# Kernel tuning notes

Measured on AMD Instinct MI355X. Metric: run time of the kernel, lower is better.

Reference implementation:

```python
import jax, jax.numpy as jnp
import numpy as np

B, N, C, O, K, D = 32, 2048, 64, 64, 3, 16

def setup_inputs() -> dict:
    key = jax.random.key(0)
    ks = jax.random.split(key, 6)
    x = jax.random.normal(ks[0], (B, N, C), dtype=jnp.float32)
    node_embeddings = jax.random.normal(ks[1], (N, D), dtype=jnp.float32)
    adj_m = jax.random.uniform(ks[2], (N, N), dtype=jnp.float32)
    weights_pool = jax.random.normal(ks[3], (D, K, C, O), dtype=jnp.float32) * 0.1
    bias_pool = jax.random.normal(ks[4], (D, O), dtype=jnp.float32) * 0.1
    sa_weight = jax.random.normal(ks[5], (N, 2 * N), dtype=jnp.float32) * (1.0 / np.sqrt(2 * N))
    return {"x": x, "node_embeddings": node_embeddings, "adj_m": adj_m,
            "weights_pool": weights_pool, "bias_pool": bias_pool, "sa_weight": sa_weight}

def reference(x, node_embeddings, adj_m, weights_pool, bias_pool, sa_weight):
    n = node_embeddings.shape[0]
    # learned adaptive adjacency [N,N]
    supports = jax.nn.softmax(jax.nn.relu(node_embeddings @ node_embeddings.T), axis=1)
    # SpatialAttention: 1x1 conv over 2N channels == matmul with [N,2N] weight
    z = jnp.concatenate([supports, adj_m], axis=1) @ sa_weight.T  # [N,N]
    s2 = jax.nn.sigmoid(z)
    supports = s2 * adj_m + (1.0 - s2) * supports
    # Chebyshev polynomial basis
    support_set = [jnp.eye(n, dtype=supports.dtype), supports]
    for _ in range(2, K):
        support_set.append(2.0 * supports @ support_set[-1] - support_set[-2])
    supports_k = jnp.stack(support_set, axis=0)  # [K,N,N]
    # per-node generated weights/bias from embeddings
    weights = jnp.einsum('nd,dkio->nkio', node_embeddings, weights_pool)  # [N,K,C,O]
    bias = node_embeddings @ bias_pool  # [N,O]
    # graph conv: aggregate then per-node matmul
    x_g = jnp.einsum('knm,bmc->bnkc', supports_k, x)  # [B,N,K,C]
    x_gconv = jnp.einsum('bnki,nkio->bno', x_g, weights) + bias  # [B,N,O]
    return x_gconv
```

## Files before the change

### kernel.cpp

```cpp
#include <hip/hip_runtime.h>


typedef unsigned short u16;
typedef float f32x4 __attribute__((ext_vector_type(4)));
typedef __bf16 bf16x8 __attribute__((ext_vector_type(8)));
typedef unsigned short u16x8 __attribute__((ext_vector_type(8)));

#define PSTRIDE ((size_t)2048 * 2048)

__device__ __forceinline__ u16 f2bf(float f) {
    unsigned u = __float_as_uint(f);
    u += 0x7FFFu + ((u >> 16) & 1u);
    return (u16)(u >> 16);
}
__device__ __forceinline__ float bf2f(u16 h) {
    return __uint_as_float((unsigned)h << 16);
}
__device__ __forceinline__ void gl_lds16(const void* g, void* l) {
    __builtin_amdgcn_global_load_lds(
        (const __attribute__((address_space(1))) unsigned*)g,
        (__attribute__((address_space(3))) unsigned*)l, 16, 0, 0);
}

__global__ __launch_bounds__(256)
void zsm(const float* __restrict__ E, u16* __restrict__ Acat) {
    __shared__ float Et[16 * 2048];
    __shared__ float redm[4][8], reds[4][8];
    const int tid = threadIdx.x;
    const int r0 = blockIdx.x * 8;

#pragma unroll
    for (int k = 0; k < 8; ++k) {
        const int n = tid + 256 * k;
        const float4* Er = (const float4*)(E + (size_t)n * 16);
        float4 e0 = Er[0], e1 = Er[1], e2 = Er[2], e3 = Er[3];
        Et[0 * 2048 + n] = e0.x;  Et[1 * 2048 + n] = e0.y;
        Et[2 * 2048 + n] = e0.z;  Et[3 * 2048 + n] = e0.w;
        Et[4 * 2048 + n] = e1.x;  Et[5 * 2048 + n] = e1.y;
        Et[6 * 2048 + n] = e1.z;  Et[7 * 2048 + n] = e1.w;
        Et[8 * 2048 + n] = e2.x;  Et[9 * 2048 + n] = e2.y;
        Et[10 * 2048 + n] = e2.z; Et[11 * 2048 + n] = e2.w;
        Et[12 * 2048 + n] = e3.x; Et[13 * 2048 + n] = e3.y;
        Et[14 * 2048 + n] = e3.z; Et[15 * 2048 + n] = e3.w;
    }
    __syncthreads();

    float z[8][8] = {};
#pragma unroll
    for (int d = 0; d < 16; ++d) {
        const float* row = Et + d * 2048;
        float ev[8];
#pragma unroll
        for (int k = 0; k < 8; ++k) ev[k] = row[tid + 256 * k];
#pragma unroll
        for (int r = 0; r < 8; ++r) {
            float e = row[r0 + r];
#pragma unroll
            for (int k = 0; k < 8; ++k) z[r][k] = fmaf(e, ev[k], z[r][k]);
        }
    }
    float mr[8];
#pragma unroll
    for (int r = 0; r < 8; ++r) {
        float m = 0.f;
#pragma unroll
        for (int k = 0; k < 8; ++k) { z[r][k] = fmaxf(z[r][k], 0.f); m = fmaxf(m, z[r][k]); }
        mr[r] = m;
    }
#pragma unroll
    for (int off = 32; off; off >>= 1)
#pragma unroll
        for (int r = 0; r < 8; ++r) mr[r] = fmaxf(mr[r], __shfl_xor(mr[r], off, 64));
    if ((tid & 63) == 0) {
#pragma unroll
        for (int r = 0; r < 8; ++r) redm[tid >> 6][r] = mr[r];
    }
    __syncthreads();
#pragma unroll
    for (int r = 0; r < 8; ++r)
        mr[r] = fmaxf(fmaxf(redm[0][r], redm[1][r]), fmaxf(redm[2][r], redm[3][r]));
    float sr[8];
#pragma unroll
    for (int r = 0; r < 8; ++r) {
        float s = 0.f;
#pragma unroll
        for (int k = 0; k < 8; ++k) { z[r][k] = __expf(z[r][k] - mr[r]); s += z[r][k]; }
        sr[r] = s;
    }
#pragma unroll
    for (int off = 32; off; off >>= 1)
#pragma unroll
        for (int r = 0; r < 8; ++r) sr[r] += __shfl_xor(sr[r], off, 64);
    if ((tid & 63) == 0) {
#pragma unroll
        for (int r = 0; r < 8; ++r) reds[tid >> 6][r] = sr[r];
    }
    __syncthreads();
#pragma unroll
    for (int r = 0; r < 8; ++r) {
        float inv = 1.f / (reds[0][r] + reds[1][r] + reds[2][r] + reds[3][r]);
        u16* orow = Acat + (size_t)(r0 + r) * 4096;
#pragma unroll
        for (int k = 0; k < 8; ++k) orow[tid + 256 * k] = f2bf(z[r][k] * inv);
    }
}

__global__ __launch_bounds__(256)
void convk(const float* __restrict__ adj, const float* __restrict__ saw,
           u16* __restrict__ Acat, u16* __restrict__ sawb) {
    const size_t NADJ = 1048576, STRIDE = (size_t)1536 * 256;
    const size_t e0 = (size_t)blockIdx.x * 256 + threadIdx.x;
    float4 v[8];
#pragma unroll
    for (int it = 0; it < 8; ++it) {
        size_t idx = e0 + (size_t)it * STRIDE;
        const float* src = (idx < NADJ) ? (adj + idx * 4) : (saw + (idx - NADJ) * 4);
        v[it] = *(const float4*)src;
    }
#pragma unroll
    for (int it = 0; it < 8; ++it) {
        size_t idx = e0 + (size_t)it * STRIDE;
        ushort4 o = make_ushort4(f2bf(v[it].x), f2bf(v[it].y), f2bf(v[it].z), f2bf(v[it].w));
        if (idx < NADJ) {
            size_t j = idx * 4;
            int n = (int)(j >> 11), c = (int)(j & 2047);
            *(ushort4*)(Acat + (size_t)n * 4096 + 2048 + c) = o;
        } else {
            *(ushort4*)(sawb + (idx - NADJ) * 4) = o;
        }
    }
}

__global__ __launch_bounds__(256)
void preamble(const float* __restrict__ E, const float* __restrict__ x,
              const float* __restrict__ Wp, const float* __restrict__ bp,
              u16* __restrict__ xtT, u16* __restrict__ Wpb, float* __restrict__ Wpbf,
              float* __restrict__ bias, u16* __restrict__ xn, int mode) {
    __shared__ float tw[64][193];
    __shared__ u16 t[64][65];
    const int bid = blockIdx.x, tid = threadIdx.x;

    if (bid < 16) {
        const int d = bid;
        const float* base = Wp + (size_t)d * 12288;
        const int o = tid & 63, seg = tid >> 6;
#pragma unroll
        for (int j = 0; j < 48; ++j) {
            int ki = seg * 48 + j;
            int k = ki >> 6, i = ki & 63;
            float v;
            if (k == 0)      v = base[i * 64 + o] - base[8192 + i * 64 + o];
            else if (k == 1) v = base[4096 + i * 64 + o];
            else             v = 2.f * base[8192 + i * 64 + o];
            tw[o][ki] = v;
        }
        __syncthreads();
#pragma unroll
        for (int it = 0; it < 12; ++it) {
            int idx = tid + it * 256;
            int oo = idx / 48, q = idx - oo * 48;
            float v0 = tw[oo][q * 4], v1 = tw[oo][q * 4 + 1];
            float v2 = tw[oo][q * 4 + 2], v3 = tw[oo][q * 4 + 3];
            size_t dst = (size_t)(d * 64 + oo) * 192 + q * 4;
            *(float4*)(Wpbf + dst) = make_float4(v0, v1, v2, v3);
            *(ushort4*)(Wpb + dst) = make_ushort4(f2bf(v0), f2bf(v1), f2bf(v2), f2bf(v3));
        }
    } else if (bid < 80) {
        const int nb = bid - 16;
#pragma unroll
        for (int it = 0; it < 8; ++it) {
            int idx = tid + it * 256;
            int n = nb * 32 + (idx >> 6), o = idx & 63;
            float s = 0.f;
#pragma unroll
            for (int d = 0; d < 16; ++d) s = fmaf(E[n * 16 + d], bp[d * 64 + o], s);
            bias[(size_t)n * 64 + o] = s;
        }
    } else {
        int local = bid - 80;
        int m0 = (local & 31) * 64, b = local >> 5;
        int c = tid & 63, g = tid >> 6;
#pragma unroll
        for (int r = 0; r < 16; ++r) {
            int mm = g * 16 + r;
            t[mm][c] = f2bf(x[((size_t)b * 2048 + m0 + mm) * 64 + c]);
        }
        __syncthreads();
#pragma unroll
        for (int r = 0; r < 16; ++r) {
            int cc = g * 16 + r;
            xtT[((size_t)b * 64 + cc) * 2048 + m0 + c] = t[c][cc];
        }
        if (mode) {
#pragma unroll
            for (int r = 0; r < 16; ++r) {
                int mm = g * 16 + r;
                xn[((size_t)(m0 + mm)) * 2048 + b * 64 + c] = t[mm][c];
            }
        }
    }
}

__global__ __launch_bounds__(256)
void mid(const float* __restrict__ E, const float* __restrict__ Wpbf,
         u16* __restrict__ Wnb) {
    __shared__ float Es[32 * 16];
    const int w = blockIdx.x, tid = threadIdx.x;
    const int c0 = (w % 12) * 1024, n0 = (w / 12) * 32;
    for (int j = tid; j < 512; j += 256) Es[j] = E[(size_t)n0 * 16 + j];
    float4 wf[16];
#pragma unroll
    for (int d = 0; d < 16; ++d)
        wf[d] = *(const float4*)(Wpbf + (size_t)d * 12288 + c0 + tid * 4);
    __syncthreads();
    for (int nl = 0; nl < 32; ++nl) {
        float4 s = make_float4(0.f, 0.f, 0.f, 0.f);
#pragma unroll
        for (int d = 0; d < 16; ++d) {
            float e = Es[nl * 16 + d];
            s.x = fmaf(e, wf[d].x, s.x);
            s.y = fmaf(e, wf[d].y, s.y);
            s.z = fmaf(e, wf[d].z, s.z);
            s.w = fmaf(e, wf[d].w, s.w);
        }
        *(ushort4*)(Wnb + (size_t)(n0 + nl) * 12288 + c0 + tid * 4) =
            make_ushort4(f2bf(s.x), f2bf(s.y), f2bf(s.z), f2bf(s.w));
    }
}

__global__ __launch_bounds__(512, 2)
void gemm_bt256(const u16* __restrict__ A, const u16* __restrict__ Bt,
                u16* __restrict__ Cp, int M, int N, int K, int Kh) {
    __shared__ alignas(16) u16 As[2][256 * 64];
    __shared__ alignas(16) u16 Bs[2][256 * 64];
    const int tid = threadIdx.x, lane = tid & 63, wave = tid >> 6;

    const int nbx = gridDim.x, nby = gridDim.y, nbz = gridDim.z;
    const int nwg = nbx * nby * nbz;
    int lin = (blockIdx.z * nby + blockIdx.y) * nbx + blockIdx.x;
    if ((nwg & 7) == 0) lin = (lin & 7) * (nwg >> 3) + (lin >> 3);
    const int bz = lin / (nbx * nby);
    const int r2 = lin - bz * nbx * nby;
    const int by = r2 / nbx, bx = r2 - by * nbx;

    const int m0 = by * 256, n0 = bx * 256;
    const int kbeg = bz * Kh;
    const int NT = Kh >> 6;
    const int wm = (wave >> 2) * 128, wn = (wave & 3) * 64;
    const int ml = lane & 15, c0l = lane >> 4;

    int sI[4], rowI[4], gcI[4];
#pragma unroll
    for (int r = 0; r < 4; ++r) {
        int s = r * 512 + tid;
        sI[r] = s; rowI[r] = s >> 3; gcI[r] = (s & 7) ^ ((s >> 3) & 7);
    }

    f32x4 acc[8][4] = {};
    bf16x8 af[4][2], bv[2][2];

#define LOADA(r_, kt_, buf_) \
    gl_lds16(A + (size_t)(m0 + rowI[r_]) * K + (kt_) + gcI[r_] * 8, \
             &As[buf_][sI[r_] * 8])
#define LOADB(r_, kt_, buf_) \
    gl_lds16(Bt + (size_t)(n0 + rowI[r_]) * K + (kt_) + gcI[r_] * 8, \
             &Bs[buf_][sI[r_] * 8])

#define DSRA(qa_) \
    _Pragma("unroll") \
    for (int i = 0; i < 4; ++i) { \
        const int mr = wm + (qa_) * 64 + i * 16 + ml; \
        _Pragma("unroll") \
        for (int ks = 0; ks < 2; ++ks) \
            af[i][ks] = *(const bf16x8*)(Asc + mr * 64 + (((c0l + ks * 4) ^ (mr & 7)) * 8)); \
    }
#define DSRB(qb_) \
    _Pragma("unroll") \
    for (int j = 0; j < 2; ++j) { \
        const int nr = wn + (qb_) * 32 + j * 16 + ml; \
        _Pragma("unroll") \
        for (int ks = 0; ks < 2; ++ks) \
            bv[j][ks] = *(const bf16x8*)(Bsc + nr * 64 + (((c0l + ks * 4) ^ (nr & 7)) * 8)); \
    }
#define MMQ(io_, jo_) \
    __builtin_amdgcn_s_barrier(); \
    asm volatile("s_waitcnt lgkmcnt(0)" ::: "memory"); \
    __builtin_amdgcn_s_setprio(1); \
    _Pragma("unroll") \
    for (int ks = 0; ks < 2; ++ks) \
        _Pragma("unroll") \
        for (int i = 0; i < 4; ++i) \
            _Pragma("unroll") \
            for (int j = 0; j < 2; ++j) \
                acc[(io_) + i][(jo_) + j] = __builtin_amdgcn_mfma_f32_16x16x32_bf16( \
                    af[i][ks], bv[j][ks], acc[(io_) + i][(jo_) + j], 0, 0, 0); \
    __builtin_amdgcn_s_setprio(0);

#pragma unroll
    for (int r = 0; r < 4; ++r) LOADA(r, kbeg, 0);
#pragma unroll
    for (int r = 0; r < 4; ++r) LOADB(r, kbeg, 0);
    asm volatile("s_waitcnt vmcnt(0)" ::: "memory");
    __builtin_amdgcn_s_barrier();

    for (int t = 0; t < NT - 1; ++t) {
        const int cur = t & 1, nxt = cur ^ 1;
        const u16* Asc = As[cur];
        const u16* Bsc = Bs[cur];
        const int k1 = kbeg + (t + 1) * 64;

        DSRA(0); DSRB(0);
        LOADB(0, k1, nxt); LOADB(1, k1, nxt);
        MMQ(0, 0);
        __builtin_amdgcn_s_barrier();

        DSRB(1);
        LOADB(2, k1, nxt); LOADB(3, k1, nxt);
        MMQ(0, 2);
        asm volatile("s_waitcnt vmcnt(4)" ::: "memory");
        __builtin_amdgcn_s_barrier();

        DSRA(1);
        LOADA(0, k1, nxt); LOADA(2, k1, nxt);
        MMQ(4, 2);
        __builtin_amdgcn_s_barrier();

        DSRB(0);
        LOADA(1, k1, nxt); LOADA(3, k1, nxt);
        MMQ(4, 0);
        asm volatile("s_waitcnt vmcnt(2)" ::: "memory");
        __builtin_amdgcn_s_barrier();
    }

    {
        const int cur = (NT - 1) & 1;
        const u16* Asc = As[cur];
        const u16* Bsc = Bs[cur];

        DSRA(0); DSRB(0);
        MMQ(0, 0);
        __builtin_amdgcn_s_barrier();

        DSRB(1);
        MMQ(0, 2);
        asm volatile("s_waitcnt vmcnt(0)" ::: "memory");
        __builtin_amdgcn_s_barrier();

        DSRA(1);
        MMQ(4, 2);
        __builtin_amdgcn_s_barrier();

        DSRB(0);
        MMQ(4, 0);
    }

#undef LOADA
#undef LOADB
#undef DSRA
#undef DSRB
#undef MMQ

    const int col_l = lane & 15, rl = (lane >> 4) * 4;
    u16* Cz = Cp + (size_t)bz * M * N;
#pragma unroll
    for (int i = 0; i < 8; ++i)
#pragma unroll
        for (int j = 0; j < 4; ++j)
#pragma unroll
            for (int r = 0; r < 4; ++r) {
                int row = m0 + wm + i * 16 + rl + r;
                int col = n0 + wn + j * 16 + col_l;
                Cz[(size_t)row * N + col] = f2bf(acc[i][j][r]);
            }
}

__global__ __launch_bounds__(256)
void reduce_z(const u16* __restrict__ p, const u16* __restrict__ Acat,
              u16* __restrict__ S) {
    const size_t base = ((size_t)blockIdx.x * 256 + threadIdx.x) * 4;
    const size_t STRIDE = (size_t)1024 * 256 * 4;
#pragma unroll
    for (int it = 0; it < 4; ++it) {
        size_t j = base + (size_t)it * STRIDE;
        ushort4 p0 = *(const ushort4*)(p + j);
        ushort4 p1 = *(const ushort4*)(p + PSTRIDE + j);
        ushort4 p2 = *(const ushort4*)(p + 2 * PSTRIDE + j);
        ushort4 p3 = *(const ushort4*)(p + 3 * PSTRIDE + j);
        int row = (int)(j >> 11), col = (int)(j & 2047);
        ushort4 sp = *(const ushort4*)(Acat + (size_t)row * 4096 + col);
        ushort4 ad = *(const ushort4*)(Acat + (size_t)row * 4096 + 2048 + col);
        float z0 = bf2f(p0.x) + bf2f(p1.x) + bf2f(p2.x) + bf2f(p3.x);
        float z1 = bf2f(p0.y) + bf2f(p1.y) + bf2f(p2.y) + bf2f(p3.y);
        float z2 = bf2f(p0.z) + bf2f(p1.z) + bf2f(p2.z) + bf2f(p3.z);
        float z3 = bf2f(p0.w) + bf2f(p1.w) + bf2f(p2.w) + bf2f(p3.w);
        float s0 = 1.f / (1.f + __expf(-z0)), s1 = 1.f / (1.f + __expf(-z1));
        float s2 = 1.f / (1.f + __expf(-z2)), s3 = 1.f / (1.f + __expf(-z3));
        ushort4 o = make_ushort4(
            f2bf(s0 * bf2f(ad.x) + (1.f - s0) * bf2f(sp.x)),
            f2bf(s1 * bf2f(ad.y) + (1.f - s1) * bf2f(sp.y)),
            f2bf(s2 * bf2f(ad.z) + (1.f - s2) * bf2f(sp.z)),
            f2bf(s3 * bf2f(ad.w) + (1.f - s3) * bf2f(sp.w)));
        *(ushort4*)(S + j) = o;
    }
}

__global__ __launch_bounds__(256)
void reduceT(const u16* __restrict__ p, u16* __restrict__ xg1o,
             u16* __restrict__ xg1T, int mode) {
    __shared__ u16 t[64][68];
    int bx = blockIdx.x * 64, by = blockIdx.y * 64;
    int cg = threadIdx.x & 15, rg = threadIdx.x >> 4;
    int b = bx >> 6;
#pragma unroll
    for (int rr = 0; rr < 4; ++rr) {
        int row = rg * 4 + rr;
        size_t idx = (size_t)(by + row) * 2048 + bx + cg * 4;
        ushort4 q0 = *(const ushort4*)(p + idx);
        ushort4 q1 = *(const ushort4*)(p + PSTRIDE + idx);
        ushort4 q2 = *(const ushort4*)(p + 2 * PSTRIDE + idx);
        ushort4 q3 = *(const ushort4*)(p + 3 * PSTRIDE + idx);
        ushort4 v = make_ushort4(
            f2bf(bf2f(q0.x) + bf2f(q1.x) + bf2f(q2.x) + bf2f(q3.x)),
            f2bf(bf2f(q0.y) + bf2f(q1.y) + bf2f(q2.y) + bf2f(q3.y)),
            f2bf(bf2f(q0.z) + bf2f(q1.z) + bf2f(q2.z) + bf2f(q3.z)),
            f2bf(bf2f(q0.w) + bf2f(q1.w) + bf2f(q2.w) + bf2f(q3.w)));
        if (mode) *(ushort4*)(xg1o + idx) = v;
        else      *(ushort4*)(xg1o + ((size_t)b * 2048 + by + row) * 64 + cg * 4) = v;
        *(ushort4*)(&t[row][cg * 4]) = v;
    }
    __syncthreads();
    int c = threadIdx.x & 63, g = threadIdx.x >> 6;
#pragma unroll
    for (int r = 0; r < 16; ++r) {
        int row = g * 16 + r;
        xg1T[(size_t)(bx + row) * 2048 + by + c] = t[c][row];
    }
}

__global__ __launch_bounds__(256, 4)
void gconv_wn(const u16* __restrict__ xn, const u16* __restrict__ xg1n,
              const u16* __restrict__ p, const u16* __restrict__ Wnb,
              const float* __restrict__ bias, float* __restrict__ out) {
    __shared__ alignas(16) u16 As[32 * 192];
    __shared__ alignas(16) u16 Bs[64 * 192];
    const int n = blockIdx.x, tid = threadIdx.x;
    const int lane = tid & 63, wave = tid >> 6;
    const int wn2 = wave * 16;
    const int ml = lane & 15, c0l = lane >> 4;
    const int col = lane & 15, rl = (lane >> 4) * 4;

#pragma unroll
    for (int it = 0; it < 6; ++it) {
        int s = tid + it * 256;
        int row = s / 24, sc = s - row * 24;
        int gc = (sc & 24) | ((sc ^ row) & 7);
        gl_lds16(Wnb + (size_t)n * 12288 + (size_t)row * 192 + gc * 8, Bs + (size_t)s * 8);
    }
#pragma unroll
    for (int it = 0; it < 3; ++it) {
        int s = tid + it * 256;
        int row = s / 24, sc = s - row * 24;
        int gc = (sc & 24) | ((sc ^ row) & 7);
        u16x8 v;
        if (gc < 8) {
            v = *(const u16x8*)(xn + (size_t)n * 2048 + row * 64 + (gc & 7) * 8);
        } else if (gc < 16) {
            v = *(const u16x8*)(xg1n + (size_t)n * 2048 + row * 64 + (gc & 7) * 8);
        } else {
            const u16* pp = p + (size_t)n * 2048 + row * 64 + (gc & 7) * 8;
            u16x8 q0 = *(const u16x8*)pp;
            u16x8 q1 = *(const u16x8*)(pp + PSTRIDE);
            u16x8 q2 = *(const u16x8*)(pp + 2 * PSTRIDE);
            u16x8 q3 = *(const u16x8*)(pp + 3 * PSTRIDE);
#pragma unroll
            for (int tt = 0; tt < 8; ++tt)
                v[tt] = f2bf(bf2f(q0[tt]) + bf2f(q1[tt]) + bf2f(q2[tt]) + bf2f(q3[tt]));
        }
        *(u16x8*)(As + (size_t)s * 8) = v;
    }
    float bv0 = bias[(size_t)n * 64 + wn2 + col];
    f32x4 acc[2];
#pragma unroll
    for (int mt = 0; mt < 2; ++mt)
#pragma unroll
        for (int r = 0; r < 4; ++r) acc[mt][r] = bv0;
    __syncthreads();

#pragma unroll
    for (int ks = 0; ks < 6; ++ks) {
        int c = c0l + ks * 4;
        int o = wn2 + ml;
        bf16x8 bfrag = *(const bf16x8*)(Bs + (o * 24 + ((c & 24) | ((c ^ (o & 7)) & 7))) * 8);
#pragma unroll
        for (int mt = 0; mt < 2; ++mt) {
            int m = mt * 16 + ml;
            bf16x8 afrag = *(const bf16x8*)(As + (m * 24 + ((c & 24) | ((c ^ (m & 7)) & 7))) * 8);
            acc[mt] = __builtin_amdgcn_mfma_f32_16x16x32_bf16(afrag, bfrag, acc[mt], 0, 0, 0);
        }
    }
#pragma unroll
    for (int mt = 0; mt < 2; ++mt)
#pragma unroll
        for (int r = 0; r < 4; ++r) {
            int b = mt * 16 + rl + r;
            out[((size_t)b * 2048 + n) * 64 + wn2 + col] = acc[mt][r];
        }
}

__global__ __launch_bounds__(256, 2)
void gconv_mfma(const float* __restrict__ x, const u16* __restrict__ xg1,
                const u16* __restrict__ p, const u16* __restrict__ Wpb,
                const float* __restrict__ bias, const float* __restrict__ E,
                float* __restrict__ out) {
    __shared__ alignas(16) float El[16 * 128];
    const int tid = threadIdx.x, lane = tid & 63, wave = tid >> 6;
    const int m0 = blockIdx.x * 128, nb = m0 & 2047, bB = m0 >> 11;
    const int wm = (wave >> 1) * 64, wn = (wave & 1) * 32;
    const int ml = lane & 15, c0l = lane >> 4;
    const int col_l = lane & 15, rl = (lane >> 4) * 4;

#pragma unroll
    for (int it = 0; it < 8; ++it) {
        int idx = tid + it * 256;
        El[idx] = E[(size_t)(nb + (idx & 127)) * 16 + (idx >> 7)];
    }
    __syncthreads();

    bf16x8 af[4][6];
#pragma unroll
    for (int i = 0; i < 4; ++i) {
        const int row = m0 + wm + i * 16 + ml;
        const int n = row & 2047;
#pragma unroll
        for (int ks = 0; ks < 2; ++ks) {
            const float* xp = x + (size_t)row * 64 + (c0l + ks * 4) * 8;
            float4 a = *(const float4*)xp, b4 = *(const float4*)(xp + 4);
            u16x8 v;
            v[0] = f2bf(a.x);  v[1] = f2bf(a.y);  v[2] = f2bf(a.z);  v[3] = f2bf(a.w);
            v[4] = f2bf(b4.x); v[5] = f2bf(b4.y); v[6] = f2bf(b4.z); v[7] = f2bf(b4.w);
            af[i][ks] = __builtin_bit_cast(bf16x8, v);
        }
#pragma unroll
        for (int ks = 2; ks < 4; ++ks)
            af[i][ks] = *(const bf16x8*)(xg1 + (size_t)row * 64 + (c0l + ks * 4 - 8) * 8);
#pragma unroll
        for (int ks = 4; ks < 6; ++ks) {
            const u16* pp = p + (size_t)n * 2048 + bB * 64 + (c0l + ks * 4 - 16) * 8;
            u16x8 q0 = *(const u16x8*)pp;
            u16x8 q1 = *(const u16x8*)(pp + PSTRIDE);
            u16x8 q2 = *(const u16x8*)(pp + 2 * PSTRIDE);
            u16x8 q3 = *(const u16x8*)(pp + 3 * PSTRIDE);
            u16x8 v;
#pragma unroll
            for (int tt = 0; tt < 8; ++tt)
                v[tt] = f2bf(bf2f(q0[tt]) + bf2f(q1[tt]) + bf2f(q2[tt]) + bf2f(q3[tt]));
            af[i][ks] = __builtin_bit_cast(bf16x8, v);
        }
    }

    f32x4 oacc[4][2];
#pragma unroll
    for (int i = 0; i < 4; ++i)
#pragma unroll
        for (int j = 0; j < 2; ++j)
#pragma unroll
            for (int r = 0; r < 4; ++r)
                oacc[i][j][r] = bias[(size_t)(nb + wm + i * 16 + rl + r) * 64 + wn + j * 16 + col_l];

#pragma unroll 2
    for (int d = 0; d < 16; ++d) {
        bf16x8 bv[2][6];
#pragma unroll
        for (int j = 0; j < 2; ++j) {
            const u16* wp = Wpb + (size_t)(d * 64 + wn + j * 16 + ml) * 192 + c0l * 8;
#pragma unroll
            for (int ks = 0; ks < 6; ++ks)
                bv[j][ks] = *(const bf16x8*)(wp + ks * 32);
        }
        f32x4 tmp[4][2] = {};
#pragma unroll
        for (int ks = 0; ks < 6; ++ks)
#pragma unroll
            for (int i = 0; i < 4; ++i)
#pragma unroll
                for (int j = 0; j < 2; ++j)
                    tmp[i][j] = __builtin_amdgcn_mfma_f32_16x16x32_bf16(af[i][ks], bv[j][ks], tmp[i][j], 0, 0, 0);
#pragma unroll
        for (int i = 0; i < 4; ++i) {
            f32x4 ev = *(const f32x4*)(El + d * 128 + wm + i * 16 + rl);
#pragma unroll
            for (int r = 0; r < 4; ++r)
#pragma unroll
                for (int j = 0; j < 2; ++j)
                    oacc[i][j][r] = fmaf(ev[r], tmp[i][j][r], oacc[i][j][r]);
        }
    }
#pragma unroll
    for (int i = 0; i < 4; ++i)
#pragma unroll
        for (int j = 0; j < 2; ++j)
#pragma unroll
            for (int r = 0; r < 4; ++r)
                out[(size_t)(m0 + wm + i * 16 + rl + r) * 64 + wn + j * 16 + col_l] = oacc[i][j][r];
}

extern "C" void kernel_launch(void* const* d_in, const int* in_sizes, int n_in,
                              void* d_out, int out_size, void* d_ws, size_t ws_size,
                              hipStream_t stream) {
    const float* x   = (const float*)d_in[0];
    const float* E   = (const float*)d_in[1];
    const float* adj = (const float*)d_in[2];
    const float* Wp  = (const float*)d_in[3];
    const float* bp  = (const float*)d_in[4];
    const float* saw = (const float*)d_in[5];
    float* out = (float*)d_out;

    char* ws = (char*)d_ws;
    const size_t MB = 1u << 20;
    const int wn_mode = (ws_size >= 140 * MB) ? 1 : 0;

    u16*   Acat  = (u16*)(ws);
    u16*   sawb  = (u16*)(ws + 16 * MB);
    u16*   XtT   = (u16*)(ws + 32 * MB);
    u16*   Wpb   = (u16*)(ws + 40 * MB);
    float* bias  = (float*)(ws + 41 * MB);
    float* Wpbf  = (float*)(ws + 42 * MB);
    u16*   part  = (u16*)(ws + 48 * MB);
    u16*   S_bf  = (u16*)(ws + 16 * MB);
    u16*   xg1T  = (u16*)(ws + 24 * MB);
    u16*   xg1o  = (u16*)(ws);
    u16*   xn    = (u16*)(ws + 80 * MB);
    u16*   Wnb   = (u16*)(ws + 88 * MB);

    zsm<<<256, 256, 0, stream>>>(E, Acat);
    preamble<<<1104, 256, 0, stream>>>(E, x, Wp, bp, XtT, Wpb, Wpbf, bias, xn, wn_mode);
    convk<<<1536, 256, 0, stream>>>(adj, saw, Acat, sawb);
    if (wn_mode)
        mid<<<768, 256, 0, stream>>>(E, Wpbf, Wnb);

    gemm_bt256<<<dim3(8, 8, 4), 512, 0, stream>>>(Acat, sawb, part, 2048, 2048, 4096, 1024);
    reduce_z<<<1024, 256, 0, stream>>>(part, Acat, S_bf);
    gemm_bt256<<<dim3(8, 8, 4), 512, 0, stream>>>(S_bf, XtT, part, 2048, 2048, 2048, 512);
    reduceT<<<dim3(32, 32), 256, 0, stream>>>(part, xg1o, xg1T, wn_mode);
    gemm_bt256<<<dim3(8, 8, 4), 512, 0, stream>>>(S_bf, xg1T, part, 2048, 2048, 2048, 512);

    if (wn_mode)
        gconv_wn<<<2048, 256, 0, stream>>>(xn, xg1o, part, Wnb, bias, out);
    else
        gconv_mfma<<<512, 256, 0, stream>>>(x, xg1o, part, Wpb, bias, E, out);
}
```

Baseline: 286.7 us.

## Merge preprocessing kernels into one launch and fold weight generation into reduce

Combines the zsm, convk and preamble kernels into a single block-indexed launch, and moves the per-node weight generation (mid) into the reduce_z launch as extra blocks. This removes several kernel launches and lets the independent work overlap on the device. The zsm branch now loads embeddings into shared memory in two 8-dim phases so that all branches fit in one 64KB shared buffer. In exchange, the fused kernel's occupancy is set by its largest shared-memory branch, and the mid work now waits until after the first GEMM.

```diff
diff --git a/kernel.cpp b/kernel.cpp
--- a/kernel.cpp
+++ b/kernel.cpp
@@ -23,125 +23,143 @@
 }
 
 __global__ __launch_bounds__(256)
-void zsm(const float* __restrict__ E, u16* __restrict__ Acat) {
-    __shared__ float Et[16 * 2048];
-    __shared__ float redm[4][8], reds[4][8];
-    const int tid = threadIdx.x;
-    const int r0 = blockIdx.x * 8;
-
-#pragma unroll
-    for (int k = 0; k < 8; ++k) {
-        const int n = tid + 256 * k;
-        const float4* Er = (const float4*)(E + (size_t)n * 16);
-        float4 e0 = Er[0], e1 = Er[1], e2 = Er[2], e3 = Er[3];
-        Et[0 * 2048 + n] = e0.x;  Et[1 * 2048 + n] = e0.y;
-        Et[2 * 2048 + n] = e0.z;  Et[3 * 2048 + n] = e0.w;
-        Et[4 * 2048 + n] = e1.x;  Et[5 * 2048 + n] = e1.y;
-        Et[6 * 2048 + n] = e1.z;  Et[7 * 2048 + n] = e1.w;
-        Et[8 * 2048 + n] = e2.x;  Et[9 * 2048 + n] = e2.y;
-        Et[10 * 2048 + n] = e2.z; Et[11 * 2048 + n] = e2.w;
-        Et[12 * 2048 + n] = e3.x; Et[13 * 2048 + n] = e3.y;
-        Et[14 * 2048 + n] = e3.z; Et[15 * 2048 + n] = e3.w;
-    }
-    __syncthreads();
-
-    float z[8][8] = {};
-#pragma unroll
-    for (int d = 0; d < 16; ++d) {
-        const float* row = Et + d * 2048;
-        float ev[8];
-#pragma unroll
-        for (int k = 0; k < 8; ++k) ev[k] = row[tid + 256 * k];
+void preA(const float* __restrict__ E, const float* __restrict__ adj,
+          const float* __restrict__ saw, const float* __restrict__ x,
+          const float* __restrict__ Wp, const float* __restrict__ bp,
+          u16* __restrict__ Acat, u16* __restrict__ sawb, u16* __restrict__ xtT,
+          u16* __restrict__ Wpb, float* __restrict__ Wpbf,
+          float* __restrict__ bias, u16* __restrict__ xn, int mode) {
+    __shared__ __align__(16) char smem[65536];
+    const int bid = blockIdx.x, tid = threadIdx.x;
+
+    if (bid < 256) {
+        float* Et8 = (float*)smem;
+        const int r0 = bid * 8;
+        float z[8][8] = {};
+#pragma unroll
+        for (int ph = 0; ph < 2; ++ph) {
+            if (ph) __syncthreads();
+#pragma unroll
+            for (int k = 0; k < 8; ++k) {
+                const int n = tid + 256 * k;
+                const float4* Er = (const float4*)(E + (size_t)n * 16) + ph * 2;
+                float4 e0 = Er[0], e1 = Er[1];
+                Et8[0 * 2048 + n] = e0.x; Et8[1 * 2048 + n] = e0.y;
+                Et8[2 * 2048 + n] = e0.z; Et8[3 * 2048 + n] = e0.w;
+                Et8[4 * 2048 + n] = e1.x; Et8[5 * 2048 + n] = e1.y;
+                Et8[6 * 2048 + n] = e1.z; Et8[7 * 2048 + n] = e1.w;
+            }
+            __syncthreads();
+#pragma unroll
+            for (int d = 0; d < 8; ++d) {
+                const float* row = Et8 + d * 2048;
+                float ev[8];
+#pragma unroll
+                for (int k = 0; k < 8; ++k) ev[k] = row[tid + 256 * k];
+#pragma unroll
+                for (int r = 0; r < 8; ++r) {
+                    float e = row[r0 + r];
+#pragma unroll
+                    for (int k = 0; k < 8; ++k) z[r][k] = fmaf(e, ev[k], z[r][k]);
+                }
+            }
+        }
+        __syncthreads();
+        float (*redm)[8] = (float(*)[8])smem;
+        float (*reds)[8] = (float(*)[8])(smem + 256);
+
+        float mr[8];
 #pragma unroll
         for (int r = 0; r < 8; ++r) {
-            float e = row[r0 + r];
-#pragma unroll
-            for (int k = 0; k < 8; ++k) z[r][k] = fmaf(e, ev[k], z[r][k]);
-        }
-    }
-    float mr[8];
-#pragma unroll
-    for (int r = 0; r < 8; ++r) {
-        float m = 0.f;
-#pragma unroll
-        for (int k = 0; k < 8; ++k) { z[r][k] = fmaxf(z[r][k], 0.f); m = fmaxf(m, z[r][k]); }
-        mr[r] = m;
-    }
-#pragma unroll
-    for (int off = 32; off; off >>= 1)
-#pragma unroll
-        for (int r = 0; r < 8; ++r) mr[r] = fmaxf(mr[r], __shfl_xor(mr[r], off, 64));
-    if ((tid & 63) == 0) {
-#pragma unroll
-        for (int r = 0; r < 8; ++r) redm[tid >> 6][r] = mr[r];
-    }
-    __syncthreads();
-#pragma unroll
-    for (int r = 0; r < 8; ++r)
-        mr[r] = fmaxf(fmaxf(redm[0][r], redm[1][r]), fmaxf(redm[2][r], redm[3][r]));
-    float sr[8];
-#pragma unroll
-    for (int r = 0; r < 8; ++r) {
-        float s = 0.f;
-#pragma unroll
-        for (int k = 0; k < 8; ++k) { z[r][k] = __expf(z[r][k] - mr[r]); s += z[r][k]; }
-        sr[r] = s;
-    }
-#pragma unroll
-    for (int off = 32; off; off >>= 1)
-#pragma unroll
-        for (int r = 0; r < 8; ++r) sr[r] += __shfl_xor(sr[r], off, 64);
-    if ((tid & 63) == 0) {
-#pragma unroll
-        for (int r = 0; r < 8; ++r) reds[tid >> 6][r] = sr[r];
-    }
-    __syncthreads();
-#pragma unroll
-    for (int r = 0; r < 8; ++r) {
-        float inv = 1.f / (reds[0][r] + reds[1][r] + reds[2][r] + reds[3][r]);
-        u16* orow = Acat + (size_t)(r0 + r) * 4096;
-#pragma unroll
-        for (int k = 0; k < 8; ++k) orow[tid + 256 * k] = f2bf(z[r][k] * inv);
-    }
-}
-
-__global__ __launch_bounds__(256)
-void convk(const float* __restrict__ adj, const float* __restrict__ saw,
-           u16* __restrict__ Acat, u16* __restrict__ sawb) {
-    const size_t NADJ = 1048576, STRIDE = (size_t)1536 * 256;
-    const size_t e0 = (size_t)blockIdx.x * 256 + threadIdx.x;
-    float4 v[8];
-#pragma unroll
-    for (int it = 0; it < 8; ++it) {
-        size_t idx = e0 + (size_t)it * STRIDE;
-        const float* src = (idx < NADJ) ? (adj + idx * 4) : (saw + (idx - NADJ) * 4);
-        v[it] = *(const float4*)src;
-    }
-#pragma unroll
-    for (int it = 0; it < 8; ++it) {
-        size_t idx = e0 + (size_t)it * STRIDE;
-        ushort4 o = make_ushort4(f2bf(v[it].x), f2bf(v[it].y), f2bf(v[it].z), f2bf(v[it].w));
-        if (idx < NADJ) {
-            size_t j = idx * 4;
-            int n = (int)(j >> 11), c = (int)(j & 2047);
-            *(ushort4*)(Acat + (size_t)n * 4096 + 2048 + c) = o;
-        } else {
-            *(ushort4*)(sawb + (idx - NADJ) * 4) = o;
-        }
-    }
-}
-
-__global__ __launch_bounds__(256)
-void preamble(const float* __restrict__ E, const float* __restrict__ x,
-              const float* __restrict__ Wp, const float* __restrict__ bp,
-              u16* __restrict__ xtT, u16* __restrict__ Wpb, float* __restrict__ Wpbf,
-              float* __restrict__ bias, u16* __restrict__ xn, int mode) {
-    __shared__ float tw[64][193];
-    __shared__ u16 t[64][65];
-    const int bid = blockIdx.x, tid = threadIdx.x;
-
-    if (bid < 16) {
-        const int d = bid;
+            float m = 0.f;
+#pragma unroll
+            for (int k = 0; k < 8; ++k) { z[r][k] = fmaxf(z[r][k], 0.f); m = fmaxf(m, z[r][k]); }
+            mr[r] = m;
+        }
+#pragma unroll
+        for (int off = 32; off; off >>= 1)
+#pragma unroll
+            for (int r = 0; r < 8; ++r) mr[r] = fmaxf(mr[r], __shfl_xor(mr[r], off, 64));
+        if ((tid & 63) == 0) {
+#pragma unroll
+            for (int r = 0; r < 8; ++r) redm[tid >> 6][r] = mr[r];
+        }
+        __syncthreads();
+#pragma unroll
+        for (int r = 0; r < 8; ++r)
+            mr[r] = fmaxf(fmaxf(redm[0][r], redm[1][r]), fmaxf(redm[2][r], redm[3][r]));
+        float sr[8];
+#pragma unroll
+        for (int r = 0; r < 8; ++r) {
+            float s = 0.f;
+#pragma unroll
+            for (int k = 0; k < 8; ++k) { z[r][k] = __expf(z[r][k] - mr[r]); s += z[r][k]; }
+            sr[r] = s;
+        }
+#pragma unroll
+        for (int off = 32; off; off >>= 1)
+#pragma unroll
+            for (int r = 0; r < 8; ++r) sr[r] += __shfl_xor(sr[r], off, 64);
+        if ((tid & 63) == 0) {
+#pragma unroll
+            for (int r = 0; r < 8; ++r) reds[tid >> 6][r] = sr[r];
+        }
+        __syncthreads();
+#pragma unroll
+        for (int r = 0; r < 8; ++r) {
+            float inv = 1.f / (reds[0][r] + reds[1][r] + reds[2][r] + reds[3][r]);
+            u16* orow = Acat + (size_t)(r0 + r) * 4096;
+#pragma unroll
+            for (int k = 0; k < 8; ++k) orow[tid + 256 * k] = f2bf(z[r][k] * inv);
+        }
+    } else if (bid < 1792) {
+        const size_t NADJ = 1048576, STRIDE = (size_t)1536 * 256;
+        const size_t e0 = (size_t)(bid - 256) * 256 + tid;
+        float4 v[8];
+#pragma unroll
+        for (int it = 0; it < 8; ++it) {
+            size_t idx = e0 + (size_t)it * STRIDE;
+            const float* src = (idx < NADJ) ? (adj + idx * 4) : (saw + (idx - NADJ) * 4);
+            v[it] = *(const float4*)src;
+        }
+#pragma unroll
+        for (int it = 0; it < 8; ++it) {
+            size_t idx = e0 + (size_t)it * STRIDE;
+            ushort4 o = make_ushort4(f2bf(v[it].x), f2bf(v[it].y), f2bf(v[it].z), f2bf(v[it].w));
+            if (idx < NADJ) {
+                size_t j = idx * 4;
+                int n = (int)(j >> 11), c = (int)(j & 2047);
+                *(ushort4*)(Acat + (size_t)n * 4096 + 2048 + c) = o;
+            } else {
+                *(ushort4*)(sawb + (idx - NADJ) * 4) = o;
+            }
+        }
+    } else if (bid < 2816) {
+        u16 (*t)[65] = (u16(*)[65])smem;
+        int local = bid - 1792;
+        int m0 = (local & 31) * 64, b = local >> 5;
+        int c = tid & 63, g = tid >> 6;
+#pragma unroll
+        for (int r = 0; r < 16; ++r) {
+            int mm = g * 16 + r;
+            t[mm][c] = f2bf(x[((size_t)b * 2048 + m0 + mm) * 64 + c]);
+        }
+        __syncthreads();
+#pragma unroll
+        for (int r = 0; r < 16; ++r) {
+            int cc = g * 16 + r;
+            xtT[((size_t)b * 64 + cc) * 2048 + m0 + c] = t[c][cc];
+        }
+        if (mode) {
+#pragma unroll
+            for (int r = 0; r < 16; ++r) {
+                int mm = g * 16 + r;
+                xn[((size_t)(m0 + mm)) * 2048 + b * 64 + c] = t[mm][c];
+            }
+        }
+    } else if (bid < 2832) {
+        float (*tw)[193] = (float(*)[193])smem;
+        const int d = bid - 2816;
         const float* base = Wp + (size_t)d * 12288;
         const int o = tid & 63, seg = tid >> 6;
 #pragma unroll
@@ -165,8 +183,8 @@
             *(float4*)(Wpbf + dst) = make_float4(v0, v1, v2, v3);
             *(ushort4*)(Wpb + dst) = make_ushort4(f2bf(v0), f2bf(v1), f2bf(v2), f2bf(v3));
         }
-    } else if (bid < 80) {
-        const int nb = bid - 16;
+    } else {
+        const int nb = bid - 2832;
 #pragma unroll
         for (int it = 0; it < 8; ++it) {
             int idx = tid + it * 256;
@@ -176,55 +194,63 @@
             for (int d = 0; d < 16; ++d) s = fmaf(E[n * 16 + d], bp[d * 64 + o], s);
             bias[(size_t)n * 64 + o] = s;
         }
+    }
+}
+
+__global__ __launch_bounds__(256)
+void rzmid(const u16* __restrict__ p, const u16* __restrict__ Acat,
+           u16* __restrict__ S, const float* __restrict__ E,
+           const float* __restrict__ Wpbf, u16* __restrict__ Wnb) {
+    __shared__ float Es[32 * 16];
+    const int bid = blockIdx.x, tid = threadIdx.x;
+    if (bid < 1024) {
+        const size_t base = ((size_t)bid * 256 + tid) * 4;
+        const size_t STRIDE = (size_t)1024 * 256 * 4;
+#pragma unroll
+        for (int it = 0; it < 4; ++it) {
+            size_t j = base + (size_t)it * STRIDE;
+            ushort4 p0 = *(const ushort4*)(p + j);
+            ushort4 p1 = *(const ushort4*)(p + PSTRIDE + j);
+            ushort4 p2 = *(const ushort4*)(p + 2 * PSTRIDE + j);
+            ushort4 p3 = *(const ushort4*)(p + 3 * PSTRIDE + j);
+            int row = (int)(j >> 11), col = (int)(j & 2047);
+            ushort4 sp = *(const ushort4*)(Acat + (size_t)row * 4096 + col);
+            ushort4 ad = *(const ushort4*)(Acat + (size_t)row * 4096 + 2048 + col);
+            float z0 = bf2f(p0.x) + bf2f(p1.x) + bf2f(p2.x) + bf2f(p3.x);
+            float z1 = bf2f(p0.y) + bf2f(p1.y) + bf2f(p2.y) + bf2f(p3.y);
+            float z2 = bf2f(p0.z) + bf2f(p1.z) + bf2f(p2.z) + bf2f(p3.z);
+            float z3 = bf2f(p0.w) + bf2f(p1.w) + bf2f(p2.w) + bf2f(p3.w);
+            float s0 = 1.f / (1.f + __expf(-z0)), s1 = 1.f / (1.f + __expf(-z1));
+            float s2 = 1.f / (1.f + __expf(-z2)), s3 = 1.f / (1.f + __expf(-z3));
+            ushort4 o = make_ushort4(
+                f2bf(s0 * bf2f(ad.x) + (1.f - s0) * bf2f(sp.x)),
+                f2bf(s1 * bf2f(ad.y) + (1.f - s1) * bf2f(sp.y)),
+                f2bf(s2 * bf2f(ad.z) + (1.f - s2) * bf2f(sp.z)),
+                f2bf(s3 * bf2f(ad.w) + (1.f - s3) * bf2f(sp.w)));
+            *(ushort4*)(S + j) = o;
+        }
     } else {
-        int local = bid - 80;
-        int m0 = (local & 31) * 64, b = local >> 5;
-        int c = tid & 63, g = tid >> 6;
-#pragma unroll
-        for (int r = 0; r < 16; ++r) {
-            int mm = g * 16 + r;
-            t[mm][c] = f2bf(x[((size_t)b * 2048 + m0 + mm) * 64 + c]);
-        }
+        const int w = bid - 1024;
+        const int c0 = (w % 12) * 1024, n0 = (w / 12) * 32;
+        for (int j = tid; j < 512; j += 256) Es[j] = E[(size_t)n0 * 16 + j];
+        float4 wf[16];
+#pragma unroll
+        for (int d = 0; d < 16; ++d)
+            wf[d] = *(const float4*)(Wpbf + (size_t)d * 12288 + c0 + tid * 4);
         __syncthreads();
-#pragma unroll
-        for (int r = 0; r < 16; ++r) {
-            int cc = g * 16 + r;
-            xtT[((size_t)b * 64 + cc) * 2048 + m0 + c] = t[c][cc];
-        }
-        if (mode) {
-#pragma unroll
-            for (int r = 0; r < 16; ++r) {
-                int mm = g * 16 + r;
-                xn[((size_t)(m0 + mm)) * 2048 + b * 64 + c] = t[mm][c];
+        for (int nl = 0; nl < 32; ++nl) {
+            float4 s = make_float4(0.f, 0.f, 0.f, 0.f);
+#pragma unroll
+            for (int d = 0; d < 16; ++d) {
+                float e = Es[nl * 16 + d];
+                s.x = fmaf(e, wf[d].x, s.x);
+                s.y = fmaf(e, wf[d].y, s.y);
+                s.z = fmaf(e, wf[d].z, s.z);
+                s.w = fmaf(e, wf[d].w, s.w);
             }
-        }
-    }
-}
-
-__global__ __launch_bounds__(256)
-void mid(const float* __restrict__ E, const float* __restrict__ Wpbf,
-         u16* __restrict__ Wnb) {
-    __shared__ float Es[32 * 16];
-    const int w = blockIdx.x, tid = threadIdx.x;
-    const int c0 = (w % 12) * 1024, n0 = (w / 12) * 32;
-    for (int j = tid; j < 512; j += 256) Es[j] = E[(size_t)n0 * 16 + j];
-    float4 wf[16];
-#pragma unroll
-    for (int d = 0; d < 16; ++d)
-        wf[d] = *(const float4*)(Wpbf + (size_t)d * 12288 + c0 + tid * 4);
-    __syncthreads();
-    for (int nl = 0; nl < 32; ++nl) {
-        float4 s = make_float4(0.f, 0.f, 0.f, 0.f);
-#pragma unroll
-        for (int d = 0; d < 16; ++d) {
-            float e = Es[nl * 16 + d];
-            s.x = fmaf(e, wf[d].x, s.x);
-            s.y = fmaf(e, wf[d].y, s.y);
-            s.z = fmaf(e, wf[d].z, s.z);
-            s.w = fmaf(e, wf[d].w, s.w);
-        }
-        *(ushort4*)(Wnb + (size_t)(n0 + nl) * 12288 + c0 + tid * 4) =
-            make_ushort4(f2bf(s.x), f2bf(s.y), f2bf(s.z), f2bf(s.w));
+            *(ushort4*)(Wnb + (size_t)(n0 + nl) * 12288 + c0 + tid * 4) =
+                make_ushort4(f2bf(s.x), f2bf(s.y), f2bf(s.z), f2bf(s.w));
+        }
     }
 }
 
@@ -372,36 +398,6 @@
                 int col = n0 + wn + j * 16 + col_l;
                 Cz[(size_t)row * N + col] = f2bf(acc[i][j][r]);
             }
-}
-
-__global__ __launch_bounds__(256)
-void reduce_z(const u16* __restrict__ p, const u16* __restrict__ Acat,
-              u16* __restrict__ S) {
-    const size_t base = ((size_t)blockIdx.x * 256 + threadIdx.x) * 4;
-    const size_t STRIDE = (size_t)1024 * 256 * 4;
-#pragma unroll
-    for (int it = 0; it < 4; ++it) {
-        size_t j = base + (size_t)it * STRIDE;
-        ushort4 p0 = *(const ushort4*)(p + j);
-        ushort4 p1 = *(const ushort4*)(p + PSTRIDE + j);
-        ushort4 p2 = *(const ushort4*)(p + 2 * PSTRIDE + j);
-        ushort4 p3 = *(const ushort4*)(p + 3 * PSTRIDE + j);
-        int row = (int)(j >> 11), col = (int)(j & 2047);
-        ushort4 sp = *(const ushort4*)(Acat + (size_t)row * 4096 + col);
-        ushort4 ad = *(const ushort4*)(Acat + (size_t)row * 4096 + 2048 + col);
-        float z0 = bf2f(p0.x) + bf2f(p1.x) + bf2f(p2.x) + bf2f(p3.x);
-        float z1 = bf2f(p0.y) + bf2f(p1.y) + bf2f(p2.y) + bf2f(p3.y);
-        float z2 = bf2f(p0.z) + bf2f(p1.z) + bf2f(p2.z) + bf2f(p3.z);
-        float z3 = bf2f(p0.w) + bf2f(p1.w) + bf2f(p2.w) + bf2f(p3.w);
-        float s0 = 1.f / (1.f + __expf(-z0)), s1 = 1.f / (1.f + __expf(-z1));
-        float s2 = 1.f / (1.f + __expf(-z2)), s3 = 1.f / (1.f + __expf(-z3));
-        ushort4 o = make_ushort4(
-            f2bf(s0 * bf2f(ad.x) + (1.f - s0) * bf2f(sp.x)),
-            f2bf(s1 * bf2f(ad.y) + (1.f - s1) * bf2f(sp.y)),
-            f2bf(s2 * bf2f(ad.z) + (1.f - s2) * bf2f(sp.z)),
-            f2bf(s3 * bf2f(ad.w) + (1.f - s3) * bf2f(sp.w)));
-        *(ushort4*)(S + j) = o;
-    }
 }
 
 __global__ __launch_bounds__(256)
@@ -632,14 +628,11 @@
     u16*   xn    = (u16*)(ws + 80 * MB);
     u16*   Wnb   = (u16*)(ws + 88 * MB);
 
-    zsm<<<256, 256, 0, stream>>>(E, Acat);
-    preamble<<<1104, 256, 0, stream>>>(E, x, Wp, bp, XtT, Wpb, Wpbf, bias, xn, wn_mode);
-    convk<<<1536, 256, 0, stream>>>(adj, saw, Acat, sawb);
-    if (wn_mode)
-        mid<<<768, 256, 0, stream>>>(E, Wpbf, Wnb);
+    preA<<<2896, 256, 0, stream>>>(E, adj, saw, x, Wp, bp, Acat, sawb, XtT,
+                                   Wpb, Wpbf, bias, xn, wn_mode);
 
     gemm_bt256<<<dim3(8, 8, 4), 512, 0, stream>>>(Acat, sawb, part, 2048, 2048, 4096, 1024);
-    reduce_z<<<1024, 256, 0, stream>>>(part, Acat, S_bf);
+    rzmid<<<wn_mode ? 1792 : 1024, 256, 0, stream>>>(part, Acat, S_bf, E, Wpbf, Wnb);
     gemm_bt256<<<dim3(8, 8, 4), 512, 0, stream>>>(S_bf, XtT, part, 2048, 2048, 2048, 512);
     reduceT<<<dim3(32, 32), 256, 0, stream>>>(part, xg1o, xg1T, wn_mode);
     gemm_bt256<<<dim3(8, 8, 4), 512, 0, stream>>>(S_bf, xg1T, part, 2048, 2048, 2048, 512);
```

Measured after the change: 278.4 us. 2.9% less time.
